# Kernel optimization log

Hardware: AMD Instinct MI355X
Metric: run time of the kernel (lower is better)

Reference implementation:

```python
import jax, jax.numpy as jnp
import numpy as np

N_NODES = 100000
N_EDGES = 3200000
IN_CH = 13
HID = 64
DIMS = [(IN_CH, HID), (HID, HID), (HID, HID), (HID, 1)]


def setup_inputs() -> dict:
    key = jax.random.key(0)
    ks = jax.random.split(key, 2 + 3 * len(DIMS))
    inp = {
        "x": jax.random.normal(ks[0], (N_NODES, IN_CH), dtype=jnp.float32),
        "edge_index": jax.random.randint(ks[1], (2, N_EDGES), 0, N_NODES, dtype=jnp.int64),
    }
    for l, (din, dout) in enumerate(DIMS):
        s = 1.0 / np.sqrt(din)
        inp[f"Wl{l}"] = jax.random.uniform(ks[2 + 3 * l], (din, dout), jnp.float32, -s, s)
        inp[f"bl{l}"] = jax.random.uniform(ks[3 + 3 * l], (dout,), jnp.float32, -s, s)
        inp[f"Wr{l}"] = jax.random.uniform(ks[4 + 3 * l], (din, dout), jnp.float32, -s, s)
    return inp


def _sage_forward(x, edge_index, params):
    src, dst = edge_index[0], edge_index[1]
    # in-degree for mean aggregation (constant across layers)
    deg = jax.ops.segment_sum(jnp.ones((edge_index.shape[1],), x.dtype), dst,
                              num_segments=N_NODES)
    inv_deg = (1.0 / jnp.maximum(deg, 1.0))[:, None]  # [N,1]
    n_layers = len(params)
    for i, (Wl, bl, Wr) in enumerate(params):
        msg = x[src]  # [E, d] neighbor gather
        mean_neigh = jax.ops.segment_sum(msg, dst, num_segments=N_NODES) * inv_deg
        x = mean_neigh @ Wl + bl + x @ Wr  # lin_l(aggr) + lin_r(root)
        if i != n_layers - 1:
            x = jax.nn.relu(x)
    return x.reshape(-1)  # [N]


def reference(x, edge_index, Wl0, bl0, Wr0, Wl1, bl1, Wr1, Wl2, bl2, Wr2, Wl3, bl3, Wr3):
    params = [(Wl0, bl0, Wr0), (Wl1, bl1, Wr1), (Wl2, bl2, Wr2), (Wl3, bl3, Wr3)]
    return _sage_forward(x, edge_index, params)
```

## Files before the change

kernel.cpp:

```cpp
#include <hip/hip_runtime.h>
#include <hip/hip_fp16.h>

#define NT 256
#define NPB 256
#define MAXBUK 512
#define A3_TILE 4096
#define NSTRIP 16
#define STRIP_SH 13

typedef _Float16 half8 __attribute__((ext_vector_type(8)));
typedef float floatx4 __attribute__((ext_vector_type(4)));


__global__ __launch_bounds__(256) void bucket_hist(const int* __restrict__ ei, int E,
                                                   int* __restrict__ bcnt, int nbuk) {
    __shared__ int h[MAXBUK];
    int t = threadIdx.x;
    for (int i = t; i < MAXBUK; i += 256) h[i] = 0;
    __syncthreads();
    const int* dsts = ei + E;
    int i0 = blockIdx.x * 256 + t;
    int stride = gridDim.x * 256;
    if ((E & 3) == 0) {
        const int4* d4 = (const int4*)dsts;
        int n4 = E >> 2;
        for (int i = i0; i < n4; i += stride) {
            int4 v = d4[i];
            atomicAdd(&h[v.x >> 8], 1);
            atomicAdd(&h[v.y >> 8], 1);
            atomicAdd(&h[v.z >> 8], 1);
            atomicAdd(&h[v.w >> 8], 1);
        }
    } else {
        for (int e = i0; e < E; e += stride) atomicAdd(&h[dsts[e] >> 8], 1);
    }
    __syncthreads();
    for (int b = t; b < nbuk; b += 256)
        if (h[b]) atomicAdd(&bcnt[b], h[b]);
}

__global__ __launch_bounds__(512) void bucket_scan(const int* __restrict__ bcnt,
                                                   int* __restrict__ bboff, int* __restrict__ bcur,
                                                   int nbuk, int* __restrict__ csr_off, int N,
                                                   int E) {
    __shared__ int s[512];
    int t = threadIdx.x;
    s[t] = (t < nbuk) ? bcnt[t] : 0;
    __syncthreads();
    for (int off = 1; off < 512; off <<= 1) {
        int v = 0;
        if (t >= off) v = s[t - off];
        __syncthreads();
        s[t] += v;
        __syncthreads();
    }
    int excl = (t == 0) ? 0 : s[t - 1];
    if (t <= nbuk) {
        bboff[t] = excl;
        if (t < nbuk) bcur[t] = excl;
    }
    if (t == 0) csr_off[N] = E;
}

__global__ __launch_bounds__(256) void partition(const int* __restrict__ ei, int E,
                                                 int* __restrict__ bcur,
                                                 unsigned int* __restrict__ pairs) {
    __shared__ int h[MAXBUK];
    __shared__ int base[MAXBUK];
    int t = threadIdx.x;
    for (int i = t; i < MAXBUK; i += 256) h[i] = 0;
    __syncthreads();
    int e0 = blockIdx.x * A3_TILE + t * 16;
    int src[16], dst[16];
    if (((E & 3) == 0) && (e0 + 15 < E)) {
        const int4* p4s = (const int4*)(ei + e0);
        const int4* p4d = (const int4*)(ei + E + e0);
#pragma unroll
        for (int j4 = 0; j4 < 4; j4++) {
            int4 s4 = p4s[j4];
            int4 d4 = p4d[j4];
            src[j4 * 4 + 0] = s4.x; dst[j4 * 4 + 0] = d4.x;
            src[j4 * 4 + 1] = s4.y; dst[j4 * 4 + 1] = d4.y;
            src[j4 * 4 + 2] = s4.z; dst[j4 * 4 + 2] = d4.z;
            src[j4 * 4 + 3] = s4.w; dst[j4 * 4 + 3] = d4.w;
        }
    } else {
#pragma unroll
        for (int j = 0; j < 16; j++) {
            int e = e0 + j;
            if (e < E) {
                src[j] = ei[e];
                dst[j] = ei[E + e];
            } else {
                dst[j] = -1;
            }
        }
    }
#pragma unroll
    for (int j = 0; j < 16; j++)
        if (dst[j] >= 0) atomicAdd(&h[dst[j] >> 8], 1);
    __syncthreads();
    for (int b = t; b < MAXBUK; b += 256) {
        int c = h[b];
        base[b] = c ? atomicAdd(&bcur[b], c) : 0;
        h[b] = 0;
    }
    __syncthreads();
#pragma unroll
    for (int j = 0; j < 16; j++) {
        if (dst[j] >= 0) {
            int bkt = dst[j] >> 8;
            int r = atomicAdd(&h[bkt], 1);
            pairs[base[bkt] + r] = ((unsigned)(dst[j] & (NPB - 1)) << 24) | (unsigned)src[j];
        }
    }
}

__global__ __launch_bounds__(512) void build_bucket(const unsigned int* __restrict__ pairs,
                                                    const int* __restrict__ bboff,
                                                    int* __restrict__ csr_off,
                                                    int* __restrict__ csr_src,
                                                    float* __restrict__ invd, int N) {
    __shared__ int h2[NPB * NSTRIP];
    __shared__ int tsum[512];
    int b = blockIdx.x, t = threadIdx.x;
    int gb0 = bboff[b], gb1 = bboff[b + 1];
    int nb0 = b << 8;
    int nn = min(NPB, N - nb0);
    for (int i = t; i < NPB * NSTRIP; i += 512) h2[i] = 0;
    __syncthreads();
    for (int i = gb0 + t; i < gb1; i += 512) {
        unsigned p = pairs[i];
        int ld = p >> 24;
        int st = (int)((p & 0xFFFFFFu) >> STRIP_SH);
        atomicAdd(&h2[ld * NSTRIP + st], 1);
    }
    __syncthreads();
    if (t < nn) {
        int d = 0;
#pragma unroll
        for (int ss = 0; ss < NSTRIP; ss++) d += h2[t * NSTRIP + ss];
        invd[nb0 + t] = 1.0f / (float)max(d, 1);
    }
    int v[8];
    int loc = 0;
#pragma unroll
    for (int j = 0; j < 8; j++) {
        v[j] = h2[t * 8 + j];
        loc += v[j];
    }
    tsum[t] = loc;
    __syncthreads();
    for (int off = 1; off < 512; off <<= 1) {
        int xv = 0;
        if (t >= off) xv = tsum[t - off];
        __syncthreads();
        tsum[t] += xv;
        __syncthreads();
    }
    int run = (t == 0) ? 0 : tsum[t - 1];
#pragma unroll
    for (int j = 0; j < 8; j++) {
        h2[t * 8 + j] = run;
        run += v[j];
    }
    __syncthreads();
    if (t < nn) csr_off[nb0 + t] = gb0 + h2[t * NSTRIP];
    __syncthreads();
    for (int i = gb0 + t; i < gb1; i += 512) {
        unsigned p = pairs[i];
        int ld = p >> 24;
        unsigned srcv = p & 0xFFFFFFu;
        int st = (int)(srcv >> STRIP_SH);
        int pos = atomicAdd(&h2[ld * NSTRIP + st], 1);
        csr_src[gb0 + pos] = (int)srcv;
    }
}


__device__ inline void acc8(float* acc, uint4 hv) {
    const __half2* hp = reinterpret_cast<const __half2*>(&hv);
#pragma unroll
    for (int j = 0; j < 4; j++) {
        float2 f = __half22float2(hp[j]);
        acc[2 * j] += f.x;
        acc[2 * j + 1] += f.y;
    }
}

__device__ inline void acc4(float* acc, uint2 hv) {
    const __half2* hp = reinterpret_cast<const __half2*>(&hv);
#pragma unroll
    for (int j = 0; j < 2; j++) {
        float2 f = __half22float2(hp[j]);
        acc[2 * j] += f.x;
        acc[2 * j + 1] += f.y;
    }
}

__global__ void pad_x(const float* __restrict__ x, __half* __restrict__ xh,
                      __half* __restrict__ inh0, int N) {
    int i = blockIdx.x * blockDim.x + threadIdx.x;
    if (i < N * 16) {
        int n = i >> 4, c = i & 15;
        float v = (c < 13) ? x[n * 13 + c] : 0.f;
        __half h = __float2half(v);
        xh[i] = h;
        inh0[(size_t)n * 32 + 16 + c] = h;
    }
}

__global__ __launch_bounds__(512) void agg16(
    const __half* __restrict__ x16h, const int* __restrict__ off, const int* __restrict__ csr,
    const float* __restrict__ invd, __half* __restrict__ inh0, int N) {
    int t = threadIdx.x, lane = t & 63, wid = t >> 6;
    int n = blockIdx.x * 8 + wid;
    if (n >= N) return;

    int g = lane >> 2;
    int c4 = (lane & 3) * 4;
    float s = invd[n];
    int e0 = off[n], e1 = off[n + 1];

    float acc[4] = {0, 0, 0, 0};
    int e = e0;
    for (; e + 31 < e1; e += 32) {
        int s0 = csr[e + g];
        int s1 = csr[e + 16 + g];
        uint2 h0 = *(const uint2*)(x16h + (size_t)s0 * 16 + c4);
        uint2 h1 = *(const uint2*)(x16h + (size_t)s1 * 16 + c4);
        acc4(acc, h0);
        acc4(acc, h1);
    }
    if (e + 15 < e1) {
        uint2 h0 = *(const uint2*)(x16h + (size_t)csr[e + g] * 16 + c4);
        acc4(acc, h0);
        e += 16;
    }
    if (e + g < e1) {
        uint2 h0 = *(const uint2*)(x16h + (size_t)csr[e + g] * 16 + c4);
        acc4(acc, h0);
    }
#pragma unroll
    for (int o = 4; o <= 32; o <<= 1) {
#pragma unroll
        for (int j = 0; j < 4; j++) acc[j] += __shfl_xor(acc[j], o);
    }
    if (lane < 4) {
        __half2 p[2];
        p[0] = __floats2half2_rn(acc[0] * s, acc[1] * s);
        p[1] = __floats2half2_rn(acc[2] * s, acc[3] * s);
        *(uint2*)(inh0 + (size_t)n * 32 + lane * 4) = *(const uint2*)p;
    }
}

__global__ __launch_bounds__(256) void gemm0(
    const __half* __restrict__ inh0, const float* __restrict__ Wl, const float* __restrict__ bl,
    const float* __restrict__ Wr, __half* __restrict__ inh1, int N) {
    __shared__ _Float16 wt[64 * 40];
    __shared__ float bs[64];
    int t = threadIdx.x;
    for (int i = t; i < 64 * 32; i += 256) {
        int k = i >> 6, c = i & 63;
        float v;
        if (k < 16) v = (k < 13) ? Wl[k * 64 + c] : 0.f;
        else {
            int kk = k - 16;
            v = (kk < 13) ? Wr[kk * 64 + c] : 0.f;
        }
        wt[c * 40 + k] = (_Float16)v;
    }
    if (t < 64) bs[t] = bl[t];
    __syncthreads();

    int lane = t & 63, wid = t >> 6;
    int n0 = blockIdx.x * 64 + wid * 16;
    int row = lane & 15, kg = lane >> 4;

    int nrow = min(n0 + row, N - 1);
    half8 a = *(const half8*)((const _Float16*)inh0 + (size_t)nrow * 32 + kg * 8);

    floatx4 acc[4];
#pragma unroll
    for (int tt = 0; tt < 4; tt++) acc[tt] = (floatx4){0.f, 0.f, 0.f, 0.f};
#pragma unroll
    for (int tt = 0; tt < 4; tt++) {
        half8 b = *(const half8*)&wt[(tt * 16 + row) * 40 + kg * 8];
        acc[tt] = __builtin_amdgcn_mfma_f32_16x16x32_f16(a, b, acc[tt], 0, 0, 0);
    }
#pragma unroll
    for (int tt = 0; tt < 4; tt++) {
        int col = tt * 16 + row;
        float bias = bs[col];
#pragma unroll
        for (int r = 0; r < 4; r++) {
            int n = n0 + kg * 4 + r;
            if (n < N) inh1[(size_t)n * 128 + 64 + col] = __float2half(fmaxf(acc[tt][r] + bias, 0.f));
        }
    }
}

__global__ __launch_bounds__(512) void agg_mean(
    __half* __restrict__ inh, const int* __restrict__ off, const int* __restrict__ csr,
    const float* __restrict__ invd, int N) {
    int t = threadIdx.x, lane = t & 63, wid = t >> 6;
    int n = blockIdx.x * 8 + wid;
    if (n >= N) return;

    int g = lane >> 3;
    int c8 = (lane & 7) * 8;
    const __half* srcb = inh + 64;
    float s = invd[n];
    int e0 = off[n], e1 = off[n + 1];

    float acc[8] = {0, 0, 0, 0, 0, 0, 0, 0};
    int e = e0;
    for (; e + 31 < e1; e += 32) {
        int s0 = csr[e + g];
        int s1 = csr[e + 8 + g];
        int s2 = csr[e + 16 + g];
        int s3 = csr[e + 24 + g];
        uint4 h0 = *(const uint4*)(srcb + (size_t)s0 * 128 + c8);
        uint4 h1 = *(const uint4*)(srcb + (size_t)s1 * 128 + c8);
        uint4 h2 = *(const uint4*)(srcb + (size_t)s2 * 128 + c8);
        uint4 h3 = *(const uint4*)(srcb + (size_t)s3 * 128 + c8);
        acc8(acc, h0);
        acc8(acc, h1);
        acc8(acc, h2);
        acc8(acc, h3);
    }
    if (e + 15 < e1) {
        int s0 = csr[e + g];
        int s1 = csr[e + 8 + g];
        uint4 h0 = *(const uint4*)(srcb + (size_t)s0 * 128 + c8);
        uint4 h1 = *(const uint4*)(srcb + (size_t)s1 * 128 + c8);
        acc8(acc, h0);
        acc8(acc, h1);
        e += 16;
    }
    if (e + 7 < e1) {
        uint4 h0 = *(const uint4*)(srcb + (size_t)csr[e + g] * 128 + c8);
        acc8(acc, h0);
        e += 8;
    }
    if (e + g < e1) {
        uint4 h0 = *(const uint4*)(srcb + (size_t)csr[e + g] * 128 + c8);
        acc8(acc, h0);
    }
#pragma unroll
    for (int o = 8; o <= 32; o <<= 1) {
#pragma unroll
        for (int j = 0; j < 8; j++) acc[j] += __shfl_xor(acc[j], o);
    }
    if (lane < 8) {
        __half2 p[4];
#pragma unroll
        for (int j = 0; j < 4; j++)
            p[j] = __floats2half2_rn(acc[2 * j] * s, acc[2 * j + 1] * s);
        *(uint4*)(inh + (size_t)n * 128 + lane * 8) = *(const uint4*)p;
    }
}

template <int LAST>
__global__ __launch_bounds__(256) void gemm_layer(
    const __half* __restrict__ inh, const float* __restrict__ Wl, const float* __restrict__ bl,
    const float* __restrict__ Wr, __half* __restrict__ inhNext,
    const float* __restrict__ Wl3, const float* __restrict__ bl3, const float* __restrict__ Wr3,
    float* __restrict__ s3, float* __restrict__ r3, int N) {
    __shared__ _Float16 wt[64 * 136];
    __shared__ float bs[64];
    int t = threadIdx.x;
    for (int i = t; i < 8192; i += 256) {
        int k = i >> 6, c = i & 63;
        float v = (k < 64) ? Wl[k * 64 + c] : Wr[(k - 64) * 64 + c];
        wt[c * 136 + k] = (_Float16)v;
    }
    if (t < 64) bs[t] = bl[t];
    __syncthreads();

    int lane = t & 63, wid = t >> 6;
    int n0 = blockIdx.x * 64 + wid * 16;
    int row = lane & 15, kg = lane >> 4;

    int nrow = min(n0 + row, N - 1);
    const _Float16* abase = (const _Float16*)inh + (size_t)nrow * 128 + kg * 8;
    half8 a[4];
#pragma unroll
    for (int kk = 0; kk < 4; kk++) a[kk] = *(const half8*)(abase + kk * 32);

    floatx4 acc[4];
#pragma unroll
    for (int tt = 0; tt < 4; tt++) acc[tt] = (floatx4){0.f, 0.f, 0.f, 0.f};

#pragma unroll
    for (int kk = 0; kk < 4; kk++) {
#pragma unroll
        for (int tt = 0; tt < 4; tt++) {
            half8 b = *(const half8*)&wt[(tt * 16 + row) * 136 + kk * 32 + kg * 8];
            acc[tt] = __builtin_amdgcn_mfma_f32_16x16x32_f16(a[kk], b, acc[tt], 0, 0, 0);
        }
    }

    if (LAST == 0) {
#pragma unroll
        for (int tt = 0; tt < 4; tt++) {
            int col = tt * 16 + row;
            float bias = bs[col];
#pragma unroll
            for (int r = 0; r < 4; r++) {
                int n = n0 + kg * 4 + r;
                float v = fmaxf(acc[tt][r] + bias, 0.f);
                if (n < N) inhNext[(size_t)n * 128 + 64 + col] = __float2half(v);
            }
        }
    } else {
        float wl3v[4], wr3v[4];
#pragma unroll
        for (int tt = 0; tt < 4; tt++) {
            int col = tt * 16 + row;
            wl3v[tt] = Wl3[col];
            wr3v[tt] = Wr3[col];
        }
        float b3 = bl3[0];
        float sp[4], rp[4];
#pragma unroll
        for (int r = 0; r < 4; r++) {
            float spv = 0.f, rpv = 0.f;
#pragma unroll
            for (int tt = 0; tt < 4; tt++) {
                float v = fmaxf(acc[tt][r] + bs[tt * 16 + row], 0.f);
                spv += v * wl3v[tt];
                rpv += v * wr3v[tt];
            }
            sp[r] = spv;
            rp[r] = rpv;
        }
#pragma unroll
        for (int o = 1; o <= 8; o <<= 1) {
#pragma unroll
            for (int r = 0; r < 4; r++) {
                sp[r] += __shfl_xor(sp[r], o);
                rp[r] += __shfl_xor(rp[r], o);
            }
        }
        if (row == 0) {
#pragma unroll
            for (int r = 0; r < 4; r++) {
                int n = n0 + kg * 4 + r;
                if (n < N) {
                    s3[n] = sp[r];
                    r3[n] = rp[r] + b3;
                }
            }
        }
    }
}

__global__ void sage_last_scalar(
    const float* __restrict__ s3, const float* __restrict__ r3, const int* __restrict__ off,
    const int* __restrict__ csr, const float* __restrict__ invd, float* __restrict__ out, int N) {
    int n = blockIdx.x * blockDim.x + threadIdx.x;
    if (n >= N) return;
    int e0 = off[n], e1 = off[n + 1];
    float acc = 0.f;
    int e = e0;
    for (; e + 3 < e1; e += 4) {
        float a0 = s3[csr[e]], a1 = s3[csr[e + 1]], a2 = s3[csr[e + 2]], a3 = s3[csr[e + 3]];
        acc += a0 + a1 + a2 + a3;
    }
    for (; e < e1; e++) acc += s3[csr[e]];
    out[n] = acc * invd[n] + r3[n];
}


extern "C" void kernel_launch(void* const* d_in, const int* in_sizes, int n_in,
                              void* d_out, int out_size, void* d_ws, size_t ws_size,
                              hipStream_t stream) {
    const float* x0 = (const float*)d_in[0];
    const int* ei = (const int*)d_in[1];
    const float* Wl[4] = {(const float*)d_in[2], (const float*)d_in[5], (const float*)d_in[8],
                          (const float*)d_in[11]};
    const float* bl[4] = {(const float*)d_in[3], (const float*)d_in[6], (const float*)d_in[9],
                          (const float*)d_in[12]};
    const float* Wr[4] = {(const float*)d_in[4], (const float*)d_in[7], (const float*)d_in[10],
                          (const float*)d_in[13]};
    float* out = (float*)d_out;

    const int N = in_sizes[0] / 13;
    const int E = in_sizes[1] / 2;
    const int nbuk = (N + NPB - 1) / NPB;

    char* w = (char*)d_ws;
    auto carve = [&](size_t bytes) {
        void* p = (void*)w;
        w += (bytes + 255) & ~size_t(255);
        return p;
    };
    int* bcnt = (int*)carve((size_t)MAXBUK * 4);
    int* bboff = (int*)carve((size_t)(MAXBUK + 1) * 4);
    int* bcur = (int*)carve((size_t)MAXBUK * 4);
    unsigned int* pairs = (unsigned int*)carve((size_t)E * 4);
    int* csr_off = (int*)carve((size_t)(N + 1) * 4);
    int* csr_src = (int*)carve((size_t)E * 4);
    float* invd = (float*)carve((size_t)N * 4);
    __half* x16h = (__half*)carve((size_t)N * 16 * 2);
    __half* inh0 = (__half*)carve((size_t)N * 32 * 2);
    __half* inh1 = (__half*)carve((size_t)N * 128 * 2);
    __half* inh2 = (__half*)carve((size_t)N * 128 * 2);
    float* s3 = (float*)carve((size_t)N * 4);
    float* r3 = (float*)carve((size_t)N * 4);

    hipMemsetAsync(bcnt, 0, (size_t)MAXBUK * 4, stream);

    bucket_hist<<<1024, 256, 0, stream>>>(ei, E, bcnt, nbuk);
    bucket_scan<<<1, 512, 0, stream>>>(bcnt, bboff, bcur, nbuk, csr_off, N, E);
    partition<<<(E + A3_TILE - 1) / A3_TILE, 256, 0, stream>>>(ei, E, bcur, pairs);
    build_bucket<<<nbuk, 512, 0, stream>>>(pairs, bboff, csr_off, csr_src, invd, N);

    pad_x<<<(N * 16 + NT - 1) / NT, NT, 0, stream>>>(x0, x16h, inh0, N);

    int nblk8 = (N + 7) / 8;
    int gblk = (N + 63) / 64;
    agg16<<<nblk8, 512, 0, stream>>>(x16h, csr_off, csr_src, invd, inh0, N);
    gemm0<<<gblk, 256, 0, stream>>>(inh0, Wl[0], bl[0], Wr[0], inh1, N);
    agg_mean<<<nblk8, 512, 0, stream>>>(inh1, csr_off, csr_src, invd, N);
    gemm_layer<0><<<gblk, 256, 0, stream>>>(inh1, Wl[1], bl[1], Wr[1], inh2,
                                            nullptr, nullptr, nullptr, nullptr, nullptr, N);
    agg_mean<<<nblk8, 512, 0, stream>>>(inh2, csr_off, csr_src, invd, N);
    gemm_layer<1><<<gblk, 256, 0, stream>>>(inh2, Wl[2], bl[2], Wr[2], nullptr,
                                            Wl[3], bl[3], Wr[3], s3, r3, N);
    sage_last_scalar<<<(N + NT - 1) / NT, NT, 0, stream>>>(s3, r3, csr_off, csr_src, invd, out, N);
}
```

Before: 286.5 us.

## Fuse neighbor aggregation with layer GEMM via shared-memory activation tile

Merges each layer's mean-aggregation kernel with the following MFMA GEMM kernel. A 512-thread block aggregates 64 nodes into a shared-memory tile alongside their root features, then four waves run the GEMM from LDS. This removes the intermediate global write and readback of the aggregated features and one launch per layer, and shrinks the feature buffers from a 128-wide concatenated layout to compact 64-wide rows, which also makes the gather rows smaller. In exchange, only half the waves do GEMM work, the per-block weight staging is repeated over a large LDS footprint, and node loops run serially per wave, which may reduce occupancy and latency hiding in the gather.

```diff
diff --git a/kernel.cpp b/kernel.cpp
--- a/kernel.cpp
+++ b/kernel.cpp
@@ -188,7 +188,7 @@
     }
 }
 
-__device__ inline void acc4(float* acc, uint2 hv) {
+__device__ inline void acc4v(float* acc, uint2 hv) {
     const __half2* hp = reinterpret_cast<const __half2*>(&hv);
 #pragma unroll
     for (int j = 0; j < 2; j++) {
@@ -198,69 +198,24 @@
     }
 }
 
-__global__ void pad_x(const float* __restrict__ x, __half* __restrict__ xh,
-                      __half* __restrict__ inh0, int N) {
+__global__ void pad_x(const float* __restrict__ x, __half* __restrict__ xroot0, int N) {
     int i = blockIdx.x * blockDim.x + threadIdx.x;
     if (i < N * 16) {
         int n = i >> 4, c = i & 15;
         float v = (c < 13) ? x[n * 13 + c] : 0.f;
-        __half h = __float2half(v);
-        xh[i] = h;
-        inh0[(size_t)n * 32 + 16 + c] = h;
-    }
-}
-
-__global__ __launch_bounds__(512) void agg16(
-    const __half* __restrict__ x16h, const int* __restrict__ off, const int* __restrict__ csr,
-    const float* __restrict__ invd, __half* __restrict__ inh0, int N) {
-    int t = threadIdx.x, lane = t & 63, wid = t >> 6;
-    int n = blockIdx.x * 8 + wid;
-    if (n >= N) return;
-
-    int g = lane >> 2;
-    int c4 = (lane & 3) * 4;
-    float s = invd[n];
-    int e0 = off[n], e1 = off[n + 1];
-
-    float acc[4] = {0, 0, 0, 0};
-    int e = e0;
-    for (; e + 31 < e1; e += 32) {
-        int s0 = csr[e + g];
-        int s1 = csr[e + 16 + g];
-        uint2 h0 = *(const uint2*)(x16h + (size_t)s0 * 16 + c4);
-        uint2 h1 = *(const uint2*)(x16h + (size_t)s1 * 16 + c4);
-        acc4(acc, h0);
-        acc4(acc, h1);
-    }
-    if (e + 15 < e1) {
-        uint2 h0 = *(const uint2*)(x16h + (size_t)csr[e + g] * 16 + c4);
-        acc4(acc, h0);
-        e += 16;
-    }
-    if (e + g < e1) {
-        uint2 h0 = *(const uint2*)(x16h + (size_t)csr[e + g] * 16 + c4);
-        acc4(acc, h0);
-    }
-#pragma unroll
-    for (int o = 4; o <= 32; o <<= 1) {
-#pragma unroll
-        for (int j = 0; j < 4; j++) acc[j] += __shfl_xor(acc[j], o);
-    }
-    if (lane < 4) {
-        __half2 p[2];
-        p[0] = __floats2half2_rn(acc[0] * s, acc[1] * s);
-        p[1] = __floats2half2_rn(acc[2] * s, acc[3] * s);
-        *(uint2*)(inh0 + (size_t)n * 32 + lane * 4) = *(const uint2*)p;
-    }
-}
-
-__global__ __launch_bounds__(256) void gemm0(
-    const __half* __restrict__ inh0, const float* __restrict__ Wl, const float* __restrict__ bl,
-    const float* __restrict__ Wr, __half* __restrict__ inh1, int N) {
+        xroot0[i] = __float2half(v);
+    }
+}
+
+__global__ __launch_bounds__(512) void fused0(
+    const __half* __restrict__ xroot0, const int* __restrict__ off, const int* __restrict__ csr,
+    const float* __restrict__ invd, const float* __restrict__ Wl, const float* __restrict__ bl,
+    const float* __restrict__ Wr, __half* __restrict__ xroot1, int N) {
+    __shared__ _Float16 act[64 * 40];
     __shared__ _Float16 wt[64 * 40];
     __shared__ float bs[64];
     int t = threadIdx.x;
-    for (int i = t; i < 64 * 32; i += 256) {
+    for (int i = t; i < 2048; i += 512) {
         int k = i >> 6, c = i & 63;
         float v;
         if (k < 16) v = (k < 13) ? Wl[k * 64 + c] : 0.f;
@@ -271,185 +226,225 @@
         wt[c * 40 + k] = (_Float16)v;
     }
     if (t < 64) bs[t] = bl[t];
-    __syncthreads();
-
+    int n0 = blockIdx.x * 64;
+    if (t < 256) {
+        int node = t >> 2, c4 = (t & 3) * 4;
+        int n = min(n0 + node, N - 1);
+        uint2 rv = *(const uint2*)(xroot0 + (size_t)n * 16 + c4);
+        *(uint2*)&act[node * 40 + 16 + c4] = rv;
+    }
     int lane = t & 63, wid = t >> 6;
-    int n0 = blockIdx.x * 64 + wid * 16;
-    int row = lane & 15, kg = lane >> 4;
-
-    int nrow = min(n0 + row, N - 1);
-    half8 a = *(const half8*)((const _Float16*)inh0 + (size_t)nrow * 32 + kg * 8);
-
-    floatx4 acc[4];
-#pragma unroll
-    for (int tt = 0; tt < 4; tt++) acc[tt] = (floatx4){0.f, 0.f, 0.f, 0.f};
-#pragma unroll
-    for (int tt = 0; tt < 4; tt++) {
-        half8 b = *(const half8*)&wt[(tt * 16 + row) * 40 + kg * 8];
-        acc[tt] = __builtin_amdgcn_mfma_f32_16x16x32_f16(a, b, acc[tt], 0, 0, 0);
-    }
-#pragma unroll
-    for (int tt = 0; tt < 4; tt++) {
-        int col = tt * 16 + row;
-        float bias = bs[col];
-#pragma unroll
-        for (int r = 0; r < 4; r++) {
-            int n = n0 + kg * 4 + r;
-            if (n < N) inh1[(size_t)n * 128 + 64 + col] = __float2half(fmaxf(acc[tt][r] + bias, 0.f));
-        }
-    }
-}
-
-__global__ __launch_bounds__(512) void agg_mean(
-    __half* __restrict__ inh, const int* __restrict__ off, const int* __restrict__ csr,
-    const float* __restrict__ invd, int N) {
-    int t = threadIdx.x, lane = t & 63, wid = t >> 6;
-    int n = blockIdx.x * 8 + wid;
-    if (n >= N) return;
-
-    int g = lane >> 3;
-    int c8 = (lane & 7) * 8;
-    const __half* srcb = inh + 64;
-    float s = invd[n];
-    int e0 = off[n], e1 = off[n + 1];
-
-    float acc[8] = {0, 0, 0, 0, 0, 0, 0, 0};
-    int e = e0;
-    for (; e + 31 < e1; e += 32) {
-        int s0 = csr[e + g];
-        int s1 = csr[e + 8 + g];
-        int s2 = csr[e + 16 + g];
-        int s3 = csr[e + 24 + g];
-        uint4 h0 = *(const uint4*)(srcb + (size_t)s0 * 128 + c8);
-        uint4 h1 = *(const uint4*)(srcb + (size_t)s1 * 128 + c8);
-        uint4 h2 = *(const uint4*)(srcb + (size_t)s2 * 128 + c8);
-        uint4 h3 = *(const uint4*)(srcb + (size_t)s3 * 128 + c8);
-        acc8(acc, h0);
-        acc8(acc, h1);
-        acc8(acc, h2);
-        acc8(acc, h3);
-    }
-    if (e + 15 < e1) {
-        int s0 = csr[e + g];
-        int s1 = csr[e + 8 + g];
-        uint4 h0 = *(const uint4*)(srcb + (size_t)s0 * 128 + c8);
-        uint4 h1 = *(const uint4*)(srcb + (size_t)s1 * 128 + c8);
-        acc8(acc, h0);
-        acc8(acc, h1);
-        e += 16;
-    }
-    if (e + 7 < e1) {
-        uint4 h0 = *(const uint4*)(srcb + (size_t)csr[e + g] * 128 + c8);
-        acc8(acc, h0);
-        e += 8;
-    }
-    if (e + g < e1) {
-        uint4 h0 = *(const uint4*)(srcb + (size_t)csr[e + g] * 128 + c8);
-        acc8(acc, h0);
-    }
-#pragma unroll
-    for (int o = 8; o <= 32; o <<= 1) {
-#pragma unroll
-        for (int j = 0; j < 8; j++) acc[j] += __shfl_xor(acc[j], o);
-    }
-    if (lane < 8) {
-        __half2 p[4];
-#pragma unroll
-        for (int j = 0; j < 4; j++)
-            p[j] = __floats2half2_rn(acc[2 * j] * s, acc[2 * j + 1] * s);
-        *(uint4*)(inh + (size_t)n * 128 + lane * 8) = *(const uint4*)p;
+    int g = lane >> 2, c4 = (lane & 3) * 4;
+#pragma unroll 1
+    for (int rr = 0; rr < 8; rr++) {
+        int nloc = rr * 8 + wid;
+        int n = min(n0 + nloc, N - 1);
+        float sc = invd[n];
+        int e0 = off[n], e1 = off[n + 1];
+        float acc[4] = {0, 0, 0, 0};
+        int e = e0;
+        for (; e + 31 < e1; e += 32) {
+            int s0 = csr[e + g];
+            int s1 = csr[e + 16 + g];
+            uint2 h0 = *(const uint2*)(xroot0 + (size_t)s0 * 16 + c4);
+            uint2 h1 = *(const uint2*)(xroot0 + (size_t)s1 * 16 + c4);
+            acc4v(acc, h0);
+            acc4v(acc, h1);
+        }
+        if (e + 15 < e1) {
+            uint2 h0 = *(const uint2*)(xroot0 + (size_t)csr[e + g] * 16 + c4);
+            acc4v(acc, h0);
+            e += 16;
+        }
+        if (e + g < e1) {
+            uint2 h0 = *(const uint2*)(xroot0 + (size_t)csr[e + g] * 16 + c4);
+            acc4v(acc, h0);
+        }
+#pragma unroll
+        for (int o = 4; o <= 32; o <<= 1) {
+#pragma unroll
+            for (int j = 0; j < 4; j++) acc[j] += __shfl_xor(acc[j], o);
+        }
+        if (lane < 4) {
+            __half2 p[2];
+            p[0] = __floats2half2_rn(acc[0] * sc, acc[1] * sc);
+            p[1] = __floats2half2_rn(acc[2] * sc, acc[3] * sc);
+            *(uint2*)&act[nloc * 40 + lane * 4] = *(const uint2*)p;
+        }
+    }
+    __syncthreads();
+    if (wid < 4) {
+        int row = lane & 15, kg = lane >> 4;
+        half8 a = *(const half8*)&act[(wid * 16 + row) * 40 + kg * 8];
+        floatx4 ac[4];
+#pragma unroll
+        for (int tt = 0; tt < 4; tt++) ac[tt] = (floatx4){0.f, 0.f, 0.f, 0.f};
+#pragma unroll
+        for (int tt = 0; tt < 4; tt++) {
+            half8 b = *(const half8*)&wt[(tt * 16 + row) * 40 + kg * 8];
+            ac[tt] = __builtin_amdgcn_mfma_f32_16x16x32_f16(a, b, ac[tt], 0, 0, 0);
+        }
+#pragma unroll
+        for (int tt = 0; tt < 4; tt++) {
+            int col = tt * 16 + row;
+            float bias = bs[col];
+#pragma unroll
+            for (int r = 0; r < 4; r++) {
+                int n = n0 + wid * 16 + kg * 4 + r;
+                if (n < N)
+                    xroot1[(size_t)n * 64 + col] = __float2half(fmaxf(ac[tt][r] + bias, 0.f));
+            }
+        }
     }
 }
 
 template <int LAST>
-__global__ __launch_bounds__(256) void gemm_layer(
-    const __half* __restrict__ inh, const float* __restrict__ Wl, const float* __restrict__ bl,
-    const float* __restrict__ Wr, __half* __restrict__ inhNext,
+__global__ __launch_bounds__(512) void fused_layer(
+    const __half* __restrict__ xroot, const int* __restrict__ off, const int* __restrict__ csr,
+    const float* __restrict__ invd, const float* __restrict__ Wl, const float* __restrict__ bl,
+    const float* __restrict__ Wr, __half* __restrict__ xnext,
     const float* __restrict__ Wl3, const float* __restrict__ bl3, const float* __restrict__ Wr3,
     float* __restrict__ s3, float* __restrict__ r3, int N) {
+    __shared__ _Float16 act[64 * 136];
     __shared__ _Float16 wt[64 * 136];
     __shared__ float bs[64];
     int t = threadIdx.x;
-    for (int i = t; i < 8192; i += 256) {
+    for (int i = t; i < 8192; i += 512) {
         int k = i >> 6, c = i & 63;
         float v = (k < 64) ? Wl[k * 64 + c] : Wr[(k - 64) * 64 + c];
         wt[c * 136 + k] = (_Float16)v;
     }
     if (t < 64) bs[t] = bl[t];
-    __syncthreads();
-
+    int n0 = blockIdx.x * 64;
+    {
+        int node = t >> 3, cc8 = (t & 7) * 8;
+        int n = min(n0 + node, N - 1);
+        uint4 rv = *(const uint4*)(xroot + (size_t)n * 64 + cc8);
+        *(uint4*)&act[node * 136 + 64 + cc8] = rv;
+    }
     int lane = t & 63, wid = t >> 6;
-    int n0 = blockIdx.x * 64 + wid * 16;
-    int row = lane & 15, kg = lane >> 4;
-
-    int nrow = min(n0 + row, N - 1);
-    const _Float16* abase = (const _Float16*)inh + (size_t)nrow * 128 + kg * 8;
-    half8 a[4];
-#pragma unroll
-    for (int kk = 0; kk < 4; kk++) a[kk] = *(const half8*)(abase + kk * 32);
-
-    floatx4 acc[4];
-#pragma unroll
-    for (int tt = 0; tt < 4; tt++) acc[tt] = (floatx4){0.f, 0.f, 0.f, 0.f};
-
-#pragma unroll
-    for (int kk = 0; kk < 4; kk++) {
-#pragma unroll
-        for (int tt = 0; tt < 4; tt++) {
-            half8 b = *(const half8*)&wt[(tt * 16 + row) * 136 + kk * 32 + kg * 8];
-            acc[tt] = __builtin_amdgcn_mfma_f32_16x16x32_f16(a[kk], b, acc[tt], 0, 0, 0);
-        }
-    }
-
-    if (LAST == 0) {
-#pragma unroll
-        for (int tt = 0; tt < 4; tt++) {
-            int col = tt * 16 + row;
-            float bias = bs[col];
+    int g = lane >> 3, c8 = (lane & 7) * 8;
+#pragma unroll 1
+    for (int rr = 0; rr < 8; rr++) {
+        int nloc = rr * 8 + wid;
+        int n = min(n0 + nloc, N - 1);
+        float sc = invd[n];
+        int e0 = off[n], e1 = off[n + 1];
+        float acc[8] = {0, 0, 0, 0, 0, 0, 0, 0};
+        int e = e0;
+        for (; e + 31 < e1; e += 32) {
+            int s0 = csr[e + g];
+            int s1 = csr[e + 8 + g];
+            int s2 = csr[e + 16 + g];
+            int s3v = csr[e + 24 + g];
+            uint4 h0 = *(const uint4*)(xroot + (size_t)s0 * 64 + c8);
+            uint4 h1 = *(const uint4*)(xroot + (size_t)s1 * 64 + c8);
+            uint4 h2 = *(const uint4*)(xroot + (size_t)s2 * 64 + c8);
+            uint4 h3 = *(const uint4*)(xroot + (size_t)s3v * 64 + c8);
+            acc8(acc, h0);
+            acc8(acc, h1);
+            acc8(acc, h2);
+            acc8(acc, h3);
+        }
+        if (e + 15 < e1) {
+            int s0 = csr[e + g];
+            int s1 = csr[e + 8 + g];
+            uint4 h0 = *(const uint4*)(xroot + (size_t)s0 * 64 + c8);
+            uint4 h1 = *(const uint4*)(xroot + (size_t)s1 * 64 + c8);
+            acc8(acc, h0);
+            acc8(acc, h1);
+            e += 16;
+        }
+        if (e + 7 < e1) {
+            uint4 h0 = *(const uint4*)(xroot + (size_t)csr[e + g] * 64 + c8);
+            acc8(acc, h0);
+            e += 8;
+        }
+        if (e + g < e1) {
+            uint4 h0 = *(const uint4*)(xroot + (size_t)csr[e + g] * 64 + c8);
+            acc8(acc, h0);
+        }
+#pragma unroll
+        for (int o = 8; o <= 32; o <<= 1) {
+#pragma unroll
+            for (int j = 0; j < 8; j++) acc[j] += __shfl_xor(acc[j], o);
+        }
+        if (lane < 8) {
+            __half2 p[4];
+#pragma unroll
+            for (int j = 0; j < 4; j++)
+                p[j] = __floats2half2_rn(acc[2 * j] * sc, acc[2 * j + 1] * sc);
+            *(uint4*)&act[nloc * 136 + lane * 8] = *(const uint4*)p;
+        }
+    }
+    __syncthreads();
+    if (wid < 4) {
+        int row = lane & 15, kg = lane >> 4;
+        const _Float16* abase = &act[(wid * 16 + row) * 136 + kg * 8];
+        half8 a[4];
+#pragma unroll
+        for (int kk = 0; kk < 4; kk++) a[kk] = *(const half8*)(abase + kk * 32);
+        floatx4 ac[4];
+#pragma unroll
+        for (int tt = 0; tt < 4; tt++) ac[tt] = (floatx4){0.f, 0.f, 0.f, 0.f};
+#pragma unroll
+        for (int kk = 0; kk < 4; kk++) {
+#pragma unroll
+            for (int tt = 0; tt < 4; tt++) {
+                half8 b = *(const half8*)&wt[(tt * 16 + row) * 136 + kk * 32 + kg * 8];
+                ac[tt] = __builtin_amdgcn_mfma_f32_16x16x32_f16(a[kk], b, ac[tt], 0, 0, 0);
+            }
+        }
+        if (LAST == 0) {
+#pragma unroll
+            for (int tt = 0; tt < 4; tt++) {
+                int col = tt * 16 + row;
+                float bias = bs[col];
+#pragma unroll
+                for (int r = 0; r < 4; r++) {
+                    int n = n0 + wid * 16 + kg * 4 + r;
+                    if (n < N)
+                        xnext[(size_t)n * 64 + col] = __float2half(fmaxf(ac[tt][r] + bias, 0.f));
+                }
+            }
+        } else {
+            float wl3v[4], wr3v[4];
+#pragma unroll
+            for (int tt = 0; tt < 4; tt++) {
+                int col = tt * 16 + row;
+                wl3v[tt] = Wl3[col];
+                wr3v[tt] = Wr3[col];
+            }
+            float b3 = bl3[0];
+            float sp[4], rp[4];
 #pragma unroll
             for (int r = 0; r < 4; r++) {
-                int n = n0 + kg * 4 + r;
-                float v = fmaxf(acc[tt][r] + bias, 0.f);
-                if (n < N) inhNext[(size_t)n * 128 + 64 + col] = __float2half(v);
-            }
-        }
-    } else {
-        float wl3v[4], wr3v[4];
-#pragma unroll
-        for (int tt = 0; tt < 4; tt++) {
-            int col = tt * 16 + row;
-            wl3v[tt] = Wl3[col];
-            wr3v[tt] = Wr3[col];
-        }
-        float b3 = bl3[0];
-        float sp[4], rp[4];
-#pragma unroll
-        for (int r = 0; r < 4; r++) {
-            float spv = 0.f, rpv = 0.f;
-#pragma unroll
-            for (int tt = 0; tt < 4; tt++) {
-                float v = fmaxf(acc[tt][r] + bs[tt * 16 + row], 0.f);
-                spv += v * wl3v[tt];
-                rpv += v * wr3v[tt];
-            }
-            sp[r] = spv;
-            rp[r] = rpv;
-        }
-#pragma unroll
-        for (int o = 1; o <= 8; o <<= 1) {
-#pragma unroll
-            for (int r = 0; r < 4; r++) {
-                sp[r] += __shfl_xor(sp[r], o);
-                rp[r] += __shfl_xor(rp[r], o);
-            }
-        }
-        if (row == 0) {
-#pragma unroll
-            for (int r = 0; r < 4; r++) {
-                int n = n0 + kg * 4 + r;
-                if (n < N) {
-                    s3[n] = sp[r];
-                    r3[n] = rp[r] + b3;
+                float spv = 0.f, rpv = 0.f;
+#pragma unroll
+                for (int tt = 0; tt < 4; tt++) {
+                    float v = fmaxf(ac[tt][r] + bs[tt * 16 + row], 0.f);
+                    spv += v * wl3v[tt];
+                    rpv += v * wr3v[tt];
+                }
+                sp[r] = spv;
+                rp[r] = rpv;
+            }
+#pragma unroll
+            for (int o = 1; o <= 8; o <<= 1) {
+#pragma unroll
+                for (int r = 0; r < 4; r++) {
+                    sp[r] += __shfl_xor(sp[r], o);
+                    rp[r] += __shfl_xor(rp[r], o);
+                }
+            }
+            if (row == 0) {
+#pragma unroll
+                for (int r = 0; r < 4; r++) {
+                    int n = n0 + wid * 16 + kg * 4 + r;
+                    if (n < N) {
+                        s3[n] = sp[r];
+                        r3[n] = rp[r] + b3;
+                    }
                 }
             }
         }
@@ -503,10 +498,9 @@
     int* csr_off = (int*)carve((size_t)(N + 1) * 4);
     int* csr_src = (int*)carve((size_t)E * 4);
     float* invd = (float*)carve((size_t)N * 4);
-    __half* x16h = (__half*)carve((size_t)N * 16 * 2);
-    __half* inh0 = (__half*)carve((size_t)N * 32 * 2);
-    __half* inh1 = (__half*)carve((size_t)N * 128 * 2);
-    __half* inh2 = (__half*)carve((size_t)N * 128 * 2);
+    __half* xroot0 = (__half*)carve((size_t)N * 16 * 2);
+    __half* xroot1 = (__half*)carve((size_t)N * 64 * 2);
+    __half* xroot2 = (__half*)carve((size_t)N * 64 * 2);
     float* s3 = (float*)carve((size_t)N * 4);
     float* r3 = (float*)carve((size_t)N * 4);
 
@@ -517,17 +511,16 @@
     partition<<<(E + A3_TILE - 1) / A3_TILE, 256, 0, stream>>>(ei, E, bcur, pairs);
     build_bucket<<<nbuk, 512, 0, stream>>>(pairs, bboff, csr_off, csr_src, invd, N);
 
-    pad_x<<<(N * 16 + NT - 1) / NT, NT, 0, stream>>>(x0, x16h, inh0, N);
-
-    int nblk8 = (N + 7) / 8;
+    pad_x<<<(N * 16 + NT - 1) / NT, NT, 0, stream>>>(x0, xroot0, N);
+
     int gblk = (N + 63) / 64;
-    agg16<<<nblk8, 512, 0, stream>>>(x16h, csr_off, csr_src, invd, inh0, N);
-    gemm0<<<gblk, 256, 0, stream>>>(inh0, Wl[0], bl[0], Wr[0], inh1, N);
-    agg_mean<<<nblk8, 512, 0, stream>>>(inh1, csr_off, csr_src, invd, N);
-    gemm_layer<0><<<gblk, 256, 0, stream>>>(inh1, Wl[1], bl[1], Wr[1], inh2,
-                                            nullptr, nullptr, nullptr, nullptr, nullptr, N);
-    agg_mean<<<nblk8, 512, 0, stream>>>(inh2, csr_off, csr_src, invd, N);
-    gemm_layer<1><<<gblk, 256, 0, stream>>>(inh2, Wl[2], bl[2], Wr[2], nullptr,
-                                            Wl[3], bl[3], Wr[3], s3, r3, N);
+    fused0<<<gblk, 512, 0, stream>>>(xroot0, csr_off, csr_src, invd,
+                                     Wl[0], bl[0], Wr[0], xroot1, N);
+    fused_layer<0><<<gblk, 512, 0, stream>>>(xroot1, csr_off, csr_src, invd,
+                                             Wl[1], bl[1], Wr[1], xroot2,
+                                             nullptr, nullptr, nullptr, nullptr, nullptr, N);
+    fused_layer<1><<<gblk, 512, 0, stream>>>(xroot2, csr_off, csr_src, invd,
+                                             Wl[2], bl[2], Wr[2], nullptr,
+                                             Wl[3], bl[3], Wr[3], s3, r3, N);
     sage_last_scalar<<<(N + NT - 1) / NT, NT, 0, stream>>>(s3, r3, csr_off, csr_src, invd, out, N);
 }
```

Measured after the change: 273.3 us. 1.05x faster.
